# Kernel optimization log

Hardware: AMD Instinct MI355X
Metric: run time of the kernel (lower is better)

## Reference

```python
import jax, jax.numpy as jnp
import numpy as np

KH, KW, STRIDE = 5, 5, 1
RY, RX = 60, 60  # (64-5)/1+1


def setup_inputs() -> dict:
    key = jax.random.key(0)
    k1, k2, k3 = jax.random.split(key, 3)
    x = jax.random.normal(k1, (128, 3, 64, 64), dtype=jnp.float32)
    # per-position unshared weights, fan-in = C*KH*KW = 75, flatten order (C, kh, kw)
    W = jax.random.normal(k2, (RY, RX, 32, 75), dtype=jnp.float32) * (1.0 / np.sqrt(75.0))
    b = jax.random.normal(k3, (RY, RX, 32), dtype=jnp.float32) * 0.01
    return {"x": x, "W": W, "b": b}


def _extract_patches(x):
    # x: [B, C, H, W] -> patches [B, RY, RX, C*KH*KW], flatten order (C, kh, kw)
    slices = []
    for dy in range(KH):
        for dx in range(KW):
            slices.append(x[:, :, dy:dy + (RY - 1) * STRIDE + 1:STRIDE,
                              dx:dx + (RX - 1) * STRIDE + 1:STRIDE])  # [B, C, RY, RX]
    p = jnp.stack(slices, axis=2)                 # [B, C, KH*KW, RY, RX]
    p = p.transpose(0, 3, 4, 1, 2)                # [B, RY, RX, C, KH*KW]
    return p.reshape(p.shape[0], RY, RX, -1)      # [B, RY, RX, C*KH*KW]


def reference(x, W, b):
    patches = _extract_patches(x)                       # [B, RY, RX, K]
    # per-position linear: out[b,o,y,x] = sum_k patches[b,y,x,k] * W[y,x,o,k] + b[y,x,o]
    out = jnp.einsum('byxk,yxok->byxo', patches, W) + b  # [B, RY, RX, O]
    return out.transpose(0, 3, 1, 2)                     # [B, O, RY, RX]
```

## Files before the change

### kernel.cpp

```cpp
#include <hip/hip_runtime.h>
#include <hip/hip_bf16.h>


#define RY 60
#define RX 60
#define OC 32
#define BATCH 128
#define CIN 3
#define HW 64
#define XT 4
#define KP 136

typedef __attribute__((ext_vector_type(8))) short short8;
typedef __attribute__((ext_vector_type(4))) float f32x4;

__device__ __forceinline__ ushort bf16u(float f) {
    __hip_bfloat16 h = __float2bfloat16(f);
    return *reinterpret_cast<ushort*>(&h);
}
__device__ __forceinline__ unsigned pk2(float a, float b) {
    return (unsigned)bf16u(a) | ((unsigned)bf16u(b) << 16);
}

__device__ __forceinline__ void stage_w(const float* __restrict__ wpos, int tid,
                                        ushort (*__restrict__ wtb)[KP], int xj)
{
    #pragma unroll
    for (int p = 0; p < 2; ++p) {
        const int g = tid + p * 256;
        if (g < 480) {
            const int o  = g / 15;
            const int cm = g - o * 15;
            const float* s = wpos + o * 75 + cm * 5;
            const ushort h[5] = {bf16u(s[0]), bf16u(s[1]), bf16u(s[2]),
                                 bf16u(s[3]), bf16u(s[4])};
            unsigned wd[4] = {0u, 0u, 0u, 0u};
            #pragma unroll
            for (int kw = 0; kw < 5; ++kw) {
                const int ww = xj + kw;
                wd[ww >> 1] |= (unsigned)h[kw] << ((ww & 1) * 16);
            }
            *reinterpret_cast<uint4*>(&wtb[o][cm * 8]) =
                make_uint4(wd[0], wd[1], wd[2], wd[3]);
        }
    }
}

template<bool COAL>
__global__ __launch_bounds__(256, 3) void lc2d_k1(
    const float* __restrict__ x, const float* __restrict__ w,
    const float* __restrict__ bias, float* __restrict__ outp,
    float* __restrict__ tmp)
{
    __shared__ ushort pa[BATCH][KP];
    __shared__ ushort wt[2][OC][KP];

    const int tid = threadIdx.x;
    const int id  = blockIdx.x;
    const int xcd = id & 7, ii = id >> 3;
    const int lin = (xcd < 4 ? xcd * 113 : 452 + (xcd - 4) * 112) + ii;
    const int y   = lin / 15;
    const int xg  = lin - y * 15;
    const int x0  = xg * 4;
    const int pos0 = y * RX + x0;

    const int lane = tid & 63;
    const int lrow = lane & 15;
    const int lgrp = lane >> 4;
    const int wid  = tid >> 6;
    const int mbase = wid * 32;

    float bb[XT][2];
    #pragma unroll
    for (int xi = 0; xi < XT; ++xi) {
        bb[xi][0] = bias[(size_t)(pos0 + xi) * OC + lrow];
        bb[xi][1] = bias[(size_t)(pos0 + xi) * OC + 16 + lrow];
    }

    #pragma unroll
    for (int i = 0; i < 8; ++i) {
        const int r = tid + i * 256;
        if (i < 7 || r < BATCH * 15) {
            const int b  = r / 15;
            const int cm = r - b * 15;
            const int c  = cm / 5;
            const int kh = cm - c * 5;
            const float* src = x + (size_t)((b * CIN + c) * HW + (y + kh)) * HW + x0;
            const float4 v0 = *(const float4*)(src);
            const float4 v1 = *(const float4*)(src + 4);
            *reinterpret_cast<uint4*>(&pa[b][cm * 8]) =
                make_uint4(pk2(v0.x, v0.y), pk2(v0.z, v0.w),
                           pk2(v1.x, v1.y), pk2(v1.z, v1.w));
        }
    }
    if (tid < 128) {
        *reinterpret_cast<uint4*>(&pa[tid][120]) = make_uint4(0u, 0u, 0u, 0u);
        *reinterpret_cast<uint4*>(&pa[tid][128]) = make_uint4(0u, 0u, 0u, 0u);
    } else {
        const int t2  = tid - 128;
        const int buf = t2 >> 6, o = (t2 >> 1) & 31, half = t2 & 1;
        *reinterpret_cast<uint4*>(&wt[buf][o][120 + half * 8]) = make_uint4(0u, 0u, 0u, 0u);
    }
    stage_w(w + (size_t)pos0 * (OC * 75), tid, wt[0], 0);
    __syncthreads();

    short8 af[4][2];
    #pragma unroll
    for (int ks = 0; ks < 4; ++ks) {
        const int koff = ks * 32 + lgrp * 8;
        af[ks][0] = *(const short8*)&pa[mbase + lrow][koff];
        af[ks][1] = *(const short8*)&pa[mbase + 16 + lrow][koff];
    }

    #pragma unroll
    for (int xi = 0; xi < XT; ++xi) {
        const int cur = xi & 1;
        if (xi + 1 < XT)
            stage_w(w + (size_t)(pos0 + xi + 1) * (OC * 75), tid, wt[cur ^ 1], xi + 1);

        f32x4 acc[2][2];
        #pragma unroll
        for (int mt = 0; mt < 2; ++mt)
            #pragma unroll
            for (int nt = 0; nt < 2; ++nt)
                acc[mt][nt] = (f32x4){0.f, 0.f, 0.f, 0.f};

        #pragma unroll
        for (int ks = 0; ks < 4; ++ks) {
            const int koff = ks * 32 + lgrp * 8;
            const short8 bf0 = *(const short8*)&wt[cur][lrow][koff];
            const short8 bf1 = *(const short8*)&wt[cur][16 + lrow][koff];
            acc[0][0] = __builtin_amdgcn_mfma_f32_16x16x32_bf16(af[ks][0], bf0, acc[0][0], 0, 0, 0);
            acc[0][1] = __builtin_amdgcn_mfma_f32_16x16x32_bf16(af[ks][0], bf1, acc[0][1], 0, 0, 0);
            acc[1][0] = __builtin_amdgcn_mfma_f32_16x16x32_bf16(af[ks][1], bf0, acc[1][0], 0, 0, 0);
            acc[1][1] = __builtin_amdgcn_mfma_f32_16x16x32_bf16(af[ks][1], bf1, acc[1][1], 0, 0, 0);
        }

        const int pos = pos0 + xi;
        if (COAL) {
            float* tb = tmp + (size_t)pos * (BATCH * OC);
            #pragma unroll
            for (int mt = 0; mt < 2; ++mt) {
                #pragma unroll
                for (int nt = 0; nt < 2; ++nt) {
                    const int o = nt * 16 + lrow;
                    #pragma unroll
                    for (int r = 0; r < 4; ++r) {
                        const int b = mbase + mt * 16 + lgrp * 4 + r;
                        tb[b * OC + o] = acc[mt][nt][r] + bb[xi][nt];
                    }
                }
            }
        } else {
            #pragma unroll
            for (int mt = 0; mt < 2; ++mt) {
                #pragma unroll
                for (int nt = 0; nt < 2; ++nt) {
                    const int o = nt * 16 + lrow;
                    #pragma unroll
                    for (int r = 0; r < 4; ++r) {
                        const int b = mbase + mt * 16 + lgrp * 4 + r;
                        outp[(size_t)(b * OC + o) * (RY * RX) + pos] = acc[mt][nt][r] + bb[xi][nt];
                    }
                }
            }
        }
        __syncthreads();
    }
}

__global__ __launch_bounds__(256) void lc2d_k2(
    const float* __restrict__ tmp, float* __restrict__ out)
{
    __shared__ float tile[64][61];
    const int y  = blockIdx.y;
    const int cb = blockIdx.x * 64;

    for (int i = threadIdx.x; i < RX * 16; i += 256) {
        const int xx  = i >> 4;
        const int cl4 = (i & 15) * 4;
        const float4 v = *(const float4*)(tmp + (size_t)(y * RX + xx) * (BATCH * OC) + cb + cl4);
        tile[cl4][xx]     = v.x;
        tile[cl4 + 1][xx] = v.y;
        tile[cl4 + 2][xx] = v.z;
        tile[cl4 + 3][xx] = v.w;
    }
    __syncthreads();

    for (int i = threadIdx.x; i < 64 * RX; i += 256) {
        const int cl = i / RX;
        const int xx = i % RX;
        out[(size_t)(cb + cl) * (RY * RX) + y * RX + xx] = tile[cl][xx];
    }
}

extern "C" void kernel_launch(void* const* d_in, const int* in_sizes, int n_in,
                              void* d_out, int out_size, void* d_ws, size_t ws_size,
                              hipStream_t stream) {
    const float* x    = (const float*)d_in[0];
    const float* w    = (const float*)d_in[1];
    const float* bias = (const float*)d_in[2];
    float* out        = (float*)d_out;
    float* tmp        = (float*)d_ws;

    const size_t tmp_bytes = (size_t)RY * RX * BATCH * OC * sizeof(float);

    if (ws_size >= tmp_bytes) {
        lc2d_k1<true><<<900, 256, 0, stream>>>(x, w, bias, out, tmp);
        lc2d_k2<<<dim3(64, RY), 256, 0, stream>>>(tmp, out);
    } else {
        lc2d_k1<false><<<900, 256, 0, stream>>>(x, w, bias, out, tmp);
    }
}
```

Baseline: 50.09 us.

## Load weights directly into MFMA B-fragments from global, drop LDS weight staging

Removes the double-buffered shared-memory weight tiles. Each lane now reads its own weight slice from global memory, converts it to bf16, and packs it into MFMA B-operand registers, so the per-iteration __syncthreads goes away. This cuts LDS usage, and the launch bound is raised to 4 blocks per CU to gain occupancy. In exchange, every wave redundantly loads the same weights from global/L2 (four waves per block), the loads are uncoalesced scalar reads, and register pressure rises.

```diff
diff --git a/kernel.cpp b/kernel.cpp
--- a/kernel.cpp
+++ b/kernel.cpp
@@ -22,38 +22,13 @@
     return (unsigned)bf16u(a) | ((unsigned)bf16u(b) << 16);
 }
 
-__device__ __forceinline__ void stage_w(const float* __restrict__ wpos, int tid,
-                                        ushort (*__restrict__ wtb)[KP], int xj)
-{
-    #pragma unroll
-    for (int p = 0; p < 2; ++p) {
-        const int g = tid + p * 256;
-        if (g < 480) {
-            const int o  = g / 15;
-            const int cm = g - o * 15;
-            const float* s = wpos + o * 75 + cm * 5;
-            const ushort h[5] = {bf16u(s[0]), bf16u(s[1]), bf16u(s[2]),
-                                 bf16u(s[3]), bf16u(s[4])};
-            unsigned wd[4] = {0u, 0u, 0u, 0u};
-            #pragma unroll
-            for (int kw = 0; kw < 5; ++kw) {
-                const int ww = xj + kw;
-                wd[ww >> 1] |= (unsigned)h[kw] << ((ww & 1) * 16);
-            }
-            *reinterpret_cast<uint4*>(&wtb[o][cm * 8]) =
-                make_uint4(wd[0], wd[1], wd[2], wd[3]);
-        }
-    }
-}
-
 template<bool COAL>
-__global__ __launch_bounds__(256, 3) void lc2d_k1(
+__global__ __launch_bounds__(256, 4) void lc2d_k1(
     const float* __restrict__ x, const float* __restrict__ w,
     const float* __restrict__ bias, float* __restrict__ outp,
     float* __restrict__ tmp)
 {
     __shared__ ushort pa[BATCH][KP];
-    __shared__ ushort wt[2][OC][KP];
 
     const int tid = threadIdx.x;
     const int id  = blockIdx.x;
@@ -96,12 +71,7 @@
     if (tid < 128) {
         *reinterpret_cast<uint4*>(&pa[tid][120]) = make_uint4(0u, 0u, 0u, 0u);
         *reinterpret_cast<uint4*>(&pa[tid][128]) = make_uint4(0u, 0u, 0u, 0u);
-    } else {
-        const int t2  = tid - 128;
-        const int buf = t2 >> 6, o = (t2 >> 1) & 31, half = t2 & 1;
-        *reinterpret_cast<uint4*>(&wt[buf][o][120 + half * 8]) = make_uint4(0u, 0u, 0u, 0u);
-    }
-    stage_w(w + (size_t)pos0 * (OC * 75), tid, wt[0], 0);
+    }
     __syncthreads();
 
     short8 af[4][2];
@@ -112,11 +82,42 @@
         af[ks][1] = *(const short8*)&pa[mbase + 16 + lrow][koff];
     }
 
+    int woff[2][4];
+    #pragma unroll
+    for (int nt = 0; nt < 2; ++nt)
+        #pragma unroll
+        for (int ks = 0; ks < 4; ++ks)
+            woff[nt][ks] = (nt * 16 + lrow) * 75 + (ks * 4 + lgrp) * 5;
+
     #pragma unroll
     for (int xi = 0; xi < XT; ++xi) {
-        const int cur = xi & 1;
-        if (xi + 1 < XT)
-            stage_w(w + (size_t)(pos0 + xi + 1) * (OC * 75), tid, wt[cur ^ 1], xi + 1);
+        const float* wp = w + (size_t)(pos0 + xi) * (OC * 75);
+
+        float wr[2][4][5];
+        #pragma unroll
+        for (int nt = 0; nt < 2; ++nt)
+            #pragma unroll
+            for (int ks = 0; ks < 4; ++ks) {
+                const float* s = wp + woff[nt][ks];
+                #pragma unroll
+                for (int j = 0; j < 5; ++j) wr[nt][ks][j] = s[j];
+            }
+
+        short8 bfr[2][4];
+        #pragma unroll
+        for (int nt = 0; nt < 2; ++nt)
+            #pragma unroll
+            for (int ks = 0; ks < 4; ++ks) {
+                unsigned wd[4] = {0u, 0u, 0u, 0u};
+                #pragma unroll
+                for (int kw = 0; kw < 5; ++kw) {
+                    const int ws = xi + kw;
+                    wd[ws >> 1] |= (unsigned)bf16u(wr[nt][ks][kw]) << ((ws & 1) * 16);
+                }
+                union { unsigned u[4]; short8 s; } cv;
+                cv.u[0] = wd[0]; cv.u[1] = wd[1]; cv.u[2] = wd[2]; cv.u[3] = wd[3];
+                bfr[nt][ks] = cv.s;
+            }
 
         f32x4 acc[2][2];
         #pragma unroll
@@ -127,20 +128,17 @@
 
         #pragma unroll
         for (int ks = 0; ks < 4; ++ks) {
-            const int koff = ks * 32 + lgrp * 8;
-            const short8 bf0 = *(const short8*)&wt[cur][lrow][koff];
-            const short8 bf1 = *(const short8*)&wt[cur][16 + lrow][koff];
-            acc[0][0] = __builtin_amdgcn_mfma_f32_16x16x32_bf16(af[ks][0], bf0, acc[0][0], 0, 0, 0);
-            acc[0][1] = __builtin_amdgcn_mfma_f32_16x16x32_bf16(af[ks][0], bf1, acc[0][1], 0, 0, 0);
-            acc[1][0] = __builtin_amdgcn_mfma_f32_16x16x32_bf16(af[ks][1], bf0, acc[1][0], 0, 0, 0);
-            acc[1][1] = __builtin_amdgcn_mfma_f32_16x16x32_bf16(af[ks][1], bf1, acc[1][1], 0, 0, 0);
+            acc[0][0] = __builtin_amdgcn_mfma_f32_16x16x32_bf16(af[ks][0], bfr[0][ks], acc[0][0], 0, 0, 0);
+            acc[0][1] = __builtin_amdgcn_mfma_f32_16x16x32_bf16(af[ks][0], bfr[1][ks], acc[0][1], 0, 0, 0);
+            acc[1][0] = __builtin_amdgcn_mfma_f32_16x16x32_bf16(af[ks][1], bfr[0][ks], acc[1][0], 0, 0, 0);
+            acc[1][1] = __builtin_amdgcn_mfma_f32_16x16x32_bf16(af[ks][1], bfr[1][ks], acc[1][1], 0, 0, 0);
         }
 
         const int pos = pos0 + xi;
         if (COAL) {
             float* tb = tmp + (size_t)pos * (BATCH * OC);
             #pragma unroll
-            for (int mt = 0; mt < 2; ++mt) {
+            for (int mt = 0; mt < 2; ++mt)
                 #pragma unroll
                 for (int nt = 0; nt < 2; ++nt) {
                     const int o = nt * 16 + lrow;
@@ -150,10 +148,9 @@
                         tb[b * OC + o] = acc[mt][nt][r] + bb[xi][nt];
                     }
                 }
-            }
         } else {
             #pragma unroll
-            for (int mt = 0; mt < 2; ++mt) {
+            for (int mt = 0; mt < 2; ++mt)
                 #pragma unroll
                 for (int nt = 0; nt < 2; ++nt) {
                     const int o = nt * 16 + lrow;
@@ -163,9 +160,7 @@
                         outp[(size_t)(b * OC + o) * (RY * RX) + pos] = acc[mt][nt][r] + bb[xi][nt];
                     }
                 }
-            }
         }
-        __syncthreads();
     }
 }
 
```

New measurement: 55.89 us. +11.6%, slower.
